# Kernel optimization log

Measured on AMD Instinct MI355X. Metric: run time of the kernel, lower is better.

## Reference

```python
import jax, jax.numpy as jnp
import numpy as np

NUM_HEADS = 16
WIN_H, WIN_W = 7, 7
DIM = 512
N = WIN_H * WIN_W  # 49 tokens per window
B_ = 2048          # num_windows * batch
NUM_WINDOWS = 64


def _relative_pos_indices(win_h, win_w):
    ch, cw = np.meshgrid(np.arange(win_h), np.arange(win_w), indexing='ij')
    coords = np.stack([ch, cw], axis=-1).reshape(-1, 2)          # (N, 2)
    rel = coords[None, :, :] - coords[:, None, :]                # (N, N, 2)
    rel[:, :, 0] += win_h - 1
    rel[:, :, 1] += win_w - 1
    rel[:, :, 0] *= 2 * win_w - 1
    return rel.sum(-1).reshape(-1).astype(np.int32)             # (N*N,)


def setup_inputs() -> dict:
    key = jax.random.key(0)
    k1, k2, k3, k4, k5 = jax.random.split(key, 5)
    x = jax.random.normal(k1, (B_, N, DIM), dtype=jnp.float32)
    # 0 / -100 shift mask (finite stand-in for -inf; same softmax effect)
    u = jax.random.uniform(k2, (NUM_WINDOWS, N, N))
    mask = jnp.where(u < 0.2, -100.0, 0.0).astype(jnp.float32)
    qkv_w = jax.random.normal(k3, (DIM, 3 * DIM), dtype=jnp.float32) * 0.02
    qkv_b = jnp.zeros((3 * DIM,), jnp.float32)
    proj_w = jax.random.normal(k4, (DIM, DIM), dtype=jnp.float32) * 0.02
    proj_b = jnp.zeros((DIM,), jnp.float32)
    bias_table = jax.random.normal(k5, ((2 * WIN_H - 1) * (2 * WIN_W - 1), NUM_HEADS), dtype=jnp.float32) * 0.02
    rel_idx = jnp.asarray(_relative_pos_indices(WIN_H, WIN_W))
    return {"x": x, "mask": mask, "qkv_w": qkv_w, "qkv_b": qkv_b,
            "proj_w": proj_w, "proj_b": proj_b,
            "bias_table": bias_table, "rel_idx": rel_idx}


def reference(x, mask, qkv_w, qkv_b, proj_w, proj_b, bias_table, rel_idx):
    b_, n, c = x.shape
    h = NUM_HEADS
    d = c // h
    scale = d ** -0.5
    qkv = (x @ qkv_w + qkv_b).reshape(b_, n, 3, h, d)
    q, k, v = jnp.moveaxis(qkv, 2, 0)                 # each (b_, n, h, d)
    attn = jnp.einsum('bnhd,bmhd->bhnm', q * scale, k)  # (b_, h, n, n)
    # relative-position bias gather: (n*n,) -> (n, n, h) -> (h, n, n)
    bias = bias_table[rel_idx].reshape(n, n, h).transpose(2, 0, 1)
    attn = attn + bias[None]
    nw = mask.shape[0]
    attn = attn.reshape(b_ // nw, nw, h, n, n) + mask[None, :, None]
    attn = jax.nn.softmax(attn.reshape(b_, h, n, n), axis=-1)
    out = jnp.einsum('bhnm,bmhd->bnhd', attn, v).reshape(b_, n, c)
    return out @ proj_w + proj_b
```

## Files before the change

kernel.cpp:

```cpp
#include <hip/hip_runtime.h>
#include <stdint.h>

typedef __attribute__((ext_vector_type(8))) short short8;
typedef __attribute__((ext_vector_type(8))) unsigned short ushort8;
typedef __attribute__((ext_vector_type(4))) unsigned short bf16x4;
typedef __attribute__((ext_vector_type(4))) float float4_t;

#define AS1 __attribute__((address_space(1)))
#define AS3 __attribute__((address_space(3)))

__device__ __forceinline__ unsigned short f2bf(float f) {
    union { float f; unsigned u; } c; c.f = f;
    return (unsigned short)((c.u + 0x7fffu + ((c.u >> 16) & 1u)) >> 16);
}

__device__ __forceinline__ void load16_lds(const void* g, void* l) {
    __builtin_amdgcn_global_load_lds((const AS1 void*)(uintptr_t)g,
                                     (AS3 void*)(uintptr_t)l, 16, 0, 0);
}

__device__ __forceinline__ void wait_vm0_barrier() {
    asm volatile("s_waitcnt vmcnt(0)" ::: "memory");
    __builtin_amdgcn_s_barrier();
    asm volatile("" ::: "memory");
}

__global__ __launch_bounds__(256)
void cvt_x(const float4_t* __restrict__ x, unsigned short* __restrict__ xb, int n8) {
    int i = blockIdx.x * 256 + threadIdx.x;
    if (i >= n8) return;
    float4_t a = x[2 * i], b = x[2 * i + 1];
    ushort8 v;
    v[0] = f2bf(a[0]); v[1] = f2bf(a[1]); v[2] = f2bf(a[2]); v[3] = f2bf(a[3]);
    v[4] = f2bf(b[0]); v[5] = f2bf(b[1]); v[6] = f2bf(b[2]); v[7] = f2bf(b[3]);
    ((ushort8*)xb)[i] = v;
}

__global__ __launch_bounds__(256)
void prep(const float* __restrict__ qkv_w, const float* __restrict__ proj_w,
          const float* __restrict__ bias_tab, const int* __restrict__ rel_idx,
          const float* __restrict__ mask,
          unsigned short* __restrict__ qkv_wT, unsigned short* __restrict__ proj_wT,
          float* __restrict__ biasP, float* __restrict__ maskP) {
    int i = blockIdx.x * 256 + threadIdx.x;
    if (i < 786432) {
        int n = i >> 9, k = i & 511;
        qkv_wT[i] = f2bf(qkv_w[k * 1536 + n]);
    } else if (i < 1048576) {
        int j = i - 786432;
        int n = j >> 9, k = j & 511;
        proj_wT[j] = f2bf(proj_w[k * 512 + n]);
    } else if (i < 1098752) {
        int j = i - 1048576;
        int h = j / 3136, mn = j % 3136;
        int m = mn >> 6, n = mn & 63;
        biasP[j] = (n < 49) ? bias_tab[rel_idx[m * 49 + n] * 16 + h] : 0.0f;
    } else {
        int j = i - 1098752;
        int w = j / 3136, mn = j % 3136;
        int m = mn >> 6, n = mn & 63;
        maskP[j] = (n < 49) ? mask[w * 2401 + m * 49 + n] : -1e30f;
    }
}

template <int MODE>
__global__ __launch_bounds__(256)
void gemm_bt(const unsigned short* __restrict__ A, const unsigned short* __restrict__ B,
             void* __restrict__ Cv, const float* __restrict__ bias,
             int M, int N, int K, float qscale) {
    __shared__ __align__(16) unsigned short As[2][128 * 32];
    __shared__ __align__(16) unsigned short Bs[2][128 * 32];

    const int t = threadIdx.x;
    const int lane = t & 63;
    const int wave = t >> 6;
    const int col = lane & 15;
    const int quad = lane >> 4;
    const int wm = (wave & 1) * 64;
    const int wn = (wave >> 1) * 64;

    const int nwg = gridDim.x;
    const int cpx = nwg >> 3;
    const int wg = (blockIdx.x & 7) * cpx + (blockIdx.x >> 3);
    const int nbx = N >> 7;
    const int m0 = (wg / nbx) * 128;
    const int n0 = (wg % nbx) * 128;

    float4_t acc[4][4] = {};

    const int row = t >> 2;
    const int seg = t & 3;
    const unsigned short* Ag0 = A + (size_t)(m0 + row) * K + seg * 8;
    const unsigned short* Ag1 = A + (size_t)(m0 + 64 + row) * K + seg * 8;
    const unsigned short* Bg0 = B + (size_t)(n0 + row) * K + seg * 8;
    const unsigned short* Bg1 = B + (size_t)(n0 + 64 + row) * K + seg * 8;

    load16_lds(Ag0, &As[0][t * 8]);
    load16_lds(Ag1, &As[0][2048 + t * 8]);
    load16_lds(Bg0, &Bs[0][t * 8]);
    load16_lds(Bg1, &Bs[0][2048 + t * 8]);
    wait_vm0_barrier();

    int cur = 0;
    for (int kk = 0; kk < K; kk += 32) {
        if (kk + 32 < K) {
            int nb = cur ^ 1;
            load16_lds(Ag0 + kk + 32, &As[nb][t * 8]);
            load16_lds(Ag1 + kk + 32, &As[nb][2048 + t * 8]);
            load16_lds(Bg0 + kk + 32, &Bs[nb][t * 8]);
            load16_lds(Bg1 + kk + 32, &Bs[nb][2048 + t * 8]);
        }
        short8 a[4], b[4];
#pragma unroll
        for (int i = 0; i < 4; ++i)
            a[i] = *(const short8*)&As[cur][(wm + i * 16 + col) * 32 + quad * 8];
#pragma unroll
        for (int j = 0; j < 4; ++j)
            b[j] = *(const short8*)&Bs[cur][(wn + j * 16 + col) * 32 + quad * 8];
#pragma unroll
        for (int i = 0; i < 4; ++i)
#pragma unroll
            for (int j = 0; j < 4; ++j)
                acc[i][j] = __builtin_amdgcn_mfma_f32_16x16x32_bf16(b[j], a[i], acc[i][j], 0, 0, 0);

        wait_vm0_barrier();
        cur ^= 1;
    }

    if (MODE == 0) {
        unsigned short* C = (unsigned short*)Cv;
#pragma unroll
        for (int j = 0; j < 4; ++j) {
            int gc0 = n0 + wn + j * 16 + quad * 4;
            float4_t bv = *(const float4_t*)&bias[gc0];
            float sc = (gc0 < 512) ? qscale : 1.0f;
#pragma unroll
            for (int i = 0; i < 4; ++i) {
                int gr = m0 + wm + i * 16 + col;
                bf16x4 u;
#pragma unroll
                for (int r = 0; r < 4; ++r) u[r] = f2bf((acc[i][j][r] + bv[r]) * sc);
                *(bf16x4*)&C[(size_t)gr * N + gc0] = u;
            }
        }
    } else {
        float* C = (float*)Cv;
#pragma unroll
        for (int j = 0; j < 4; ++j) {
            int gc0 = n0 + wn + j * 16 + quad * 4;
            float4_t bv = *(const float4_t*)&bias[gc0];
#pragma unroll
            for (int i = 0; i < 4; ++i) {
                int gr = m0 + wm + i * 16 + col;
                float4_t ov = acc[i][j] + bv;
                *(float4_t*)&C[(size_t)gr * N + gc0] = ov;
            }
        }
    }
}

__global__ __launch_bounds__(64)
void attn_win(const unsigned short* __restrict__ qkv,
              const float* __restrict__ maskP,
              const float* __restrict__ biasP,
              unsigned short* __restrict__ attn_out) {
    __shared__ __align__(16) unsigned short P[64 * 64];
    __shared__ __align__(16) unsigned short Vt[32 * 64];

    const int bh = blockIdx.x;
    const int w = bh >> 4;
    const int hh = bh & 15;
    const int lane = threadIdx.x;
    const int col = lane & 15;
    const int quad = lane >> 4;
    const size_t rowbase = (size_t)(w * 49) * 1536;

    {
        ushort8 u0 = {}, u1 = {}, u2 = {}, u3 = {};
        if (lane < 49) {
            const ushort8* vp = (const ushort8*)(qkv + rowbase + (size_t)lane * 1536 + 1024 + hh * 32);
            u0 = vp[0]; u1 = vp[1]; u2 = vp[2]; u3 = vp[3];
        }
#pragma unroll
        for (int c = 0; c < 8; ++c) {
            Vt[((c) * 64 + lane) ^ ((c & 7) << 3)] = u0[c];
            Vt[((c + 8) * 64 + lane) ^ ((c & 7) << 3)] = u1[c];
            Vt[((c + 16) * 64 + lane) ^ ((c & 7) << 3)] = u2[c];
            Vt[((c + 24) * 64 + lane) ^ ((c & 7) << 3)] = u3[c];
        }
    }

    float4_t s[4][4] = {};
    {
        short8 qf[4], kf[4];
#pragma unroll
        for (int i = 0; i < 4; ++i) {
            int m = i * 16 + col; if (m > 48) m = 48;
            qf[i] = *(const short8*)(qkv + rowbase + (size_t)m * 1536 + hh * 32 + quad * 8);
            kf[i] = *(const short8*)(qkv + rowbase + (size_t)m * 1536 + 512 + hh * 32 + quad * 8);
        }
#pragma unroll
        for (int i = 0; i < 4; ++i)
#pragma unroll
            for (int j = 0; j < 4; ++j)
                s[i][j] = __builtin_amdgcn_mfma_f32_16x16x32_bf16(kf[j], qf[i], s[i][j], 0, 0, 0);
    }

    {
        const float* mk = maskP + (size_t)(w & 63) * 3136;
        const float* bs = biasP + (size_t)hh * 3136;
#pragma unroll
        for (int i = 0; i < 4; ++i) {
            int mc = i * 16 + col; if (mc > 48) mc = 48;
#pragma unroll
            for (int j = 0; j < 4; ++j) {
                int n0 = j * 16 + quad * 4;
                float4_t a4 = *(const float4_t*)&mk[mc * 64 + n0];
                float4_t b4 = *(const float4_t*)&bs[mc * 64 + n0];
#pragma unroll
                for (int r = 0; r < 4; ++r) s[i][j][r] += a4[r] + b4[r];
            }
        }
    }

#pragma unroll
    for (int i = 0; i < 4; ++i) {
        int m = i * 16 + col;
        float mx = s[i][0][0];
#pragma unroll
        for (int j = 0; j < 4; ++j)
#pragma unroll
            for (int r = 0; r < 4; ++r) mx = fmaxf(mx, s[i][j][r]);
        mx = fmaxf(mx, __shfl_xor(mx, 16));
        mx = fmaxf(mx, __shfl_xor(mx, 32));
        float sum = 0.f;
#pragma unroll
        for (int j = 0; j < 4; ++j)
#pragma unroll
            for (int r = 0; r < 4; ++r) {
                float e = __expf(s[i][j][r] - mx);
                s[i][j][r] = e; sum += e;
            }
        sum += __shfl_xor(sum, 16);
        sum += __shfl_xor(sum, 32);
        float inv = 1.0f / sum;
#pragma unroll
        for (int j = 0; j < 4; ++j) {
            bf16x4 u;
#pragma unroll
            for (int r = 0; r < 4; ++r) u[r] = f2bf(s[i][j][r] * inv);
            *(bf16x4*)&P[(m * 64 + j * 16 + quad * 4) ^ ((m & 7) << 3)] = u;
        }
    }
    __syncthreads();

    float4_t o[4][2] = {};
#pragma unroll
    for (int s2 = 0; s2 < 2; ++s2) {
        short8 pa[4], vb[2];
#pragma unroll
        for (int i = 0; i < 4; ++i) {
            int m = i * 16 + col;
            pa[i] = *(const short8*)&P[(m * 64 + s2 * 32 + quad * 8) ^ ((m & 7) << 3)];
        }
#pragma unroll
        for (int tj = 0; tj < 2; ++tj) {
            int d = tj * 16 + col;
            vb[tj] = *(const short8*)&Vt[(d * 64 + s2 * 32 + quad * 8) ^ ((d & 7) << 3)];
        }
#pragma unroll
        for (int i = 0; i < 4; ++i)
#pragma unroll
            for (int tj = 0; tj < 2; ++tj)
                o[i][tj] = __builtin_amdgcn_mfma_f32_16x16x32_bf16(vb[tj], pa[i], o[i][tj], 0, 0, 0);
    }

#pragma unroll
    for (int i = 0; i < 4; ++i) {
        int m = i * 16 + col;
        if (m < 49) {
            size_t ob = (size_t)(w * 49 + m) * 512 + hh * 32 + quad * 4;
#pragma unroll
            for (int tj = 0; tj < 2; ++tj) {
                bf16x4 u;
#pragma unroll
                for (int r = 0; r < 4; ++r) u[r] = f2bf(o[i][tj][r]);
                *(bf16x4*)&attn_out[ob + tj * 16] = u;
            }
        }
    }
}

extern "C" void kernel_launch(void* const* d_in, const int* in_sizes, int n_in,
                              void* d_out, int out_size, void* d_ws, size_t ws_size,
                              hipStream_t stream) {
    const float* x        = (const float*)d_in[0];
    const float* mask     = (const float*)d_in[1];
    const float* qkv_w    = (const float*)d_in[2];
    const float* qkv_b    = (const float*)d_in[3];
    const float* proj_w   = (const float*)d_in[4];
    const float* proj_b   = (const float*)d_in[5];
    const float* bias_tab = (const float*)d_in[6];
    const int*   rel_idx  = (const int*)d_in[7];
    float* out = (float*)d_out;

    char* ws = (char*)d_ws;
    size_t off = 0;
    auto carve = [&](size_t bytes) -> char* {
        char* p = ws + off;
        off += (bytes + 255) & ~(size_t)255;
        return p;
    };
    unsigned short* x_bf    = (unsigned short*)carve((size_t)51380224 * 2);
    unsigned short* qkv_wT  = (unsigned short*)carve((size_t)786432 * 2);
    unsigned short* proj_wT = (unsigned short*)carve((size_t)262144 * 2);
    float*          biasP   = (float*)carve((size_t)50176 * 4);
    float*          maskP   = (float*)carve((size_t)200704 * 4);
    unsigned short* qkv_o   = (unsigned short*)carve((size_t)100352 * 1536 * 2);
    unsigned short* attn_o  = x_bf;

    cvt_x<<<25088, 256, 0, stream>>>((const float4_t*)x, x_bf, 6422528);
    prep<<<5076, 256, 0, stream>>>(qkv_w, proj_w, bias_tab, rel_idx, mask,
                                   qkv_wT, proj_wT, biasP, maskP);
    gemm_bt<0><<<9408, 256, 0, stream>>>(x_bf, qkv_wT, (void*)qkv_o, qkv_b,
                                         100352, 1536, 512, 0.17677669529663687f);
    attn_win<<<32768, 64, 0, stream>>>(qkv_o, maskP, biasP, attn_o);
    gemm_bt<1><<<3136, 256, 0, stream>>>(attn_o, proj_wT, (void*)out, proj_b,
                                         100352, 512, 512, 1.0f);
}
```

Before: 934.5 us.

## Deepen GEMM LDS pipeline to four stages with partial vmcnt waits and setprio

Replaces the double-buffered GEMM mainloop with a 4-slot ring that keeps three tiles of global-to-LDS loads in flight. Each iteration waits only on the oldest tile's loads (vmcnt 8/4/0) and needs a single barrier instead of a full drain. It also raises wave priority around the MFMA blocks in the GEMM and attention kernels so matrix issue is favoured. The cost is doubled LDS per block (64KB), which may lower occupancy.

Measured after the change: 916.7 us. No clear change (-1.9%).

```diff
diff --git a/kernel.cpp b/kernel.cpp
--- a/kernel.cpp
+++ b/kernel.cpp
@@ -17,12 +17,6 @@
 __device__ __forceinline__ void load16_lds(const void* g, void* l) {
     __builtin_amdgcn_global_load_lds((const AS1 void*)(uintptr_t)g,
                                      (AS3 void*)(uintptr_t)l, 16, 0, 0);
-}
-
-__device__ __forceinline__ void wait_vm0_barrier() {
-    asm volatile("s_waitcnt vmcnt(0)" ::: "memory");
-    __builtin_amdgcn_s_barrier();
-    asm volatile("" ::: "memory");
 }
 
 __global__ __launch_bounds__(256)
@@ -68,8 +62,8 @@
 void gemm_bt(const unsigned short* __restrict__ A, const unsigned short* __restrict__ B,
              void* __restrict__ Cv, const float* __restrict__ bias,
              int M, int N, int K, float qscale) {
-    __shared__ __align__(16) unsigned short As[2][128 * 32];
-    __shared__ __align__(16) unsigned short Bs[2][128 * 32];
+    __shared__ __align__(16) unsigned short As[4 * 128 * 32];
+    __shared__ __align__(16) unsigned short Bs[4 * 128 * 32];
 
     const int t = threadIdx.x;
     const int lane = t & 63;
@@ -95,36 +89,44 @@
     const unsigned short* Bg0 = B + (size_t)(n0 + row) * K + seg * 8;
     const unsigned short* Bg1 = B + (size_t)(n0 + 64 + row) * K + seg * 8;
 
-    load16_lds(Ag0, &As[0][t * 8]);
-    load16_lds(Ag1, &As[0][2048 + t * 8]);
-    load16_lds(Bg0, &Bs[0][t * 8]);
-    load16_lds(Bg1, &Bs[0][2048 + t * 8]);
-    wait_vm0_barrier();
-
-    int cur = 0;
-    for (int kk = 0; kk < K; kk += 32) {
-        if (kk + 32 < K) {
-            int nb = cur ^ 1;
-            load16_lds(Ag0 + kk + 32, &As[nb][t * 8]);
-            load16_lds(Ag1 + kk + 32, &As[nb][2048 + t * 8]);
-            load16_lds(Bg0 + kk + 32, &Bs[nb][t * 8]);
-            load16_lds(Bg1 + kk + 32, &Bs[nb][2048 + t * 8]);
-        }
+    auto stage = [&](int tile) {
+        const int kk = tile << 5;
+        unsigned short* Ad = As + ((tile & 3) << 12);
+        unsigned short* Bd = Bs + ((tile & 3) << 12);
+        load16_lds(Ag0 + kk, Ad + t * 8);
+        load16_lds(Ag1 + kk, Ad + 2048 + t * 8);
+        load16_lds(Bg0 + kk, Bd + t * 8);
+        load16_lds(Bg1 + kk, Bd + 2048 + t * 8);
+    };
+
+    const int nt = K >> 5;
+    stage(0); stage(1); stage(2);
+
+    for (int tt = 0; tt < nt; ++tt) {
+        if (tt < nt - 2)       asm volatile("s_waitcnt vmcnt(8)" ::: "memory");
+        else if (tt == nt - 2) asm volatile("s_waitcnt vmcnt(4)" ::: "memory");
+        else                   asm volatile("s_waitcnt vmcnt(0)" ::: "memory");
+        __builtin_amdgcn_s_barrier();
+        asm volatile("" ::: "memory");
+
+        if (tt + 3 < nt) stage(tt + 3);
+
+        const unsigned short* Ab = As + ((size_t)(tt & 3) << 12);
+        const unsigned short* Bb = Bs + ((size_t)(tt & 3) << 12);
         short8 a[4], b[4];
 #pragma unroll
         for (int i = 0; i < 4; ++i)
-            a[i] = *(const short8*)&As[cur][(wm + i * 16 + col) * 32 + quad * 8];
+            a[i] = *(const short8*)&Ab[(wm + i * 16 + col) * 32 + quad * 8];
 #pragma unroll
         for (int j = 0; j < 4; ++j)
-            b[j] = *(const short8*)&Bs[cur][(wn + j * 16 + col) * 32 + quad * 8];
+            b[j] = *(const short8*)&Bb[(wn + j * 16 + col) * 32 + quad * 8];
+        __builtin_amdgcn_s_setprio(1);
 #pragma unroll
         for (int i = 0; i < 4; ++i)
 #pragma unroll
             for (int j = 0; j < 4; ++j)
                 acc[i][j] = __builtin_amdgcn_mfma_f32_16x16x32_bf16(b[j], a[i], acc[i][j], 0, 0, 0);
-
-        wait_vm0_barrier();
-        cur ^= 1;
+        __builtin_amdgcn_s_setprio(0);
     }
 
     if (MODE == 0) {
@@ -199,11 +201,13 @@
             qf[i] = *(const short8*)(qkv + rowbase + (size_t)m * 1536 + hh * 32 + quad * 8);
             kf[i] = *(const short8*)(qkv + rowbase + (size_t)m * 1536 + 512 + hh * 32 + quad * 8);
         }
+        __builtin_amdgcn_s_setprio(1);
 #pragma unroll
         for (int i = 0; i < 4; ++i)
 #pragma unroll
             for (int j = 0; j < 4; ++j)
                 s[i][j] = __builtin_amdgcn_mfma_f32_16x16x32_bf16(kf[j], qf[i], s[i][j], 0, 0, 0);
+        __builtin_amdgcn_s_setprio(0);
     }
 
     {
@@ -268,11 +272,13 @@
             int d = tj * 16 + col;
             vb[tj] = *(const short8*)&Vt[(d * 64 + s2 * 32 + quad * 8) ^ ((d & 7) << 3)];
         }
+        __builtin_amdgcn_s_setprio(1);
 #pragma unroll
         for (int i = 0; i < 4; ++i)
 #pragma unroll
             for (int tj = 0; tj < 2; ++tj)
                 o[i][tj] = __builtin_amdgcn_mfma_f32_16x16x32_bf16(vb[tj], pa[i], o[i][tj], 0, 0, 0);
+        __builtin_amdgcn_s_setprio(0);
     }
 
 #pragma unroll
```
